# Performance work log

Measured on AMD Instinct MI355X. Metric: run time of the kernel, lower is better.

Reference implementation:

```python
import jax, jax.numpy as jnp
import numpy as np

IOU_THR = 0.5
TOP_K = 10
D_MODEL = 256
BS, NQ = 8, 1000


def _layer_norm(x, g, b, eps=1e-5):
    m = x.mean(-1, keepdims=True)
    v = ((x - m) ** 2).mean(-1, keepdims=True)
    return (x - m) * jax.lax.rsqrt(v + eps) * g + b


def _box_iou(boxes):
    # boxes: [nq, 4] xyxy; pairwise IoU [nq, nq]
    area = (boxes[:, 2] - boxes[:, 0]) * (boxes[:, 3] - boxes[:, 1])
    lt = jnp.maximum(boxes[:, None, :2], boxes[None, :, :2])
    rb = jnp.minimum(boxes[:, None, 2:], boxes[None, :, 2:])
    wh = jnp.clip(rb - lt, 0.0)
    inter = wh[..., 0] * wh[..., 1]
    union = area[:, None] + area[None, :] - inter
    return inter / union


def setup_inputs() -> dict:
    key = jax.random.key(0)
    ks = jax.random.split(key, 16)
    d = D_MODEL
    s = 1.0 / np.sqrt(d)
    tgt = jax.random.normal(ks[0], (BS, NQ, d), dtype=jnp.float32)
    seed_mask = (jax.random.uniform(ks[1], (BS, NQ, 1)) < 0.2).astype(jnp.float32)
    # cxcywh boxes in (0,1) with positive wh
    cxy = jax.random.uniform(ks[2], (BS, NQ, 2), minval=0.1, maxval=0.9)
    wh = jax.random.uniform(ks[3], (BS, NQ, 2), minval=0.05, maxval=0.3)
    pred_boxes = jnp.concatenate([cxy, wh], axis=-1).astype(jnp.float32)
    def lin(k):
        kw, kb = jax.random.split(k)
        return (jax.random.uniform(kw, (d, d), minval=-s, maxval=s, dtype=jnp.float32),
                jax.random.uniform(kb, (d,), minval=-s, maxval=s, dtype=jnp.float32))
    W1, b1 = lin(ks[4]); W2, b2 = lin(ks[5]); W3, b3 = lin(ks[6])
    W4, b4 = lin(ks[7]); W5, b5 = lin(ks[8])
    g2 = jnp.ones((d,), jnp.float32); be2 = jnp.zeros((d,), jnp.float32)
    return {"tgt": tgt, "seed_mask": seed_mask, "pred_boxes": pred_boxes,
            "W1": W1, "b1": b1, "W2": W2, "b2": b2, "g2": g2, "be2": be2,
            "W3": W3, "b3": b3, "W4": W4, "b4": b4, "W5": W5, "b5": b5}


def reference(tgt, seed_mask, pred_boxes, W1, b1, W2, b2, g2, be2, W3, b3, W4, b4, W5, b5):
    bs, nq, d = tgt.shape
    # cxcywh -> xyxy
    cxy, wh = pred_boxes[..., :2], pred_boxes[..., 2:]
    box_xyxy = jnp.concatenate([cxy - 0.5 * wh, cxy + 0.5 * wh], axis=-1)
    ious = jax.vmap(_box_iou)(box_xyxy)                       # [bs,nq,nq]
    attn_mask = ious >= IOU_THR
    neg_mask = 1.0 - seed_mask                                # [bs,nq,1]
    # mask out non-seed columns and seed rows
    overlaps = ious * jnp.swapaxes(seed_mask, 1, 2) * neg_mask  # [bs,nq,nq]
    idx = jnp.argsort(-overlaps, axis=-1)[..., :TOP_K]        # [bs,nq,k]
    nmk = jnp.take_along_axis(
        jnp.broadcast_to(jnp.swapaxes(seed_mask, 1, 2), (bs, nq, nq)), idx, axis=2)
    ious_g = jnp.take_along_axis(overlaps, idx, axis=2)       # [bs,nq,k]
    mk = nmk * (ious_g >= IOU_THR).astype(tgt.dtype)          # [bs,nq,k]
    # id token MLP + layernorm
    id_token = _layer_norm(jax.nn.relu(tgt @ W1 + b1) @ W2 + b2, g2, be2)
    # neighbor gather: [bs,nq,k,d]
    neighbors_id = jax.vmap(lambda t, i: t[i])(id_token, idx)
    id_feature = id_token[:, :, None, :] - neighbors_id
    features = jax.nn.relu(id_feature @ W3 + b3) @ W4 + b4
    cur_tgt = (features * mk[..., None]).max(axis=2)          # [bs,nq,d]
    cur_tgt = tgt + jax.nn.relu(cur_tgt @ W5 + b5) * neg_mask
    return cur_tgt, attn_mask
```

## Files before the change

kernel.cpp:

```cpp
#include <hip/hip_runtime.h>
#include <hip/hip_bf16.h>

#define BSZ   8
#define NQ    1000
#define DM    256
#define MROWS (BSZ*NQ)
#define TOPK  10

typedef __attribute__((ext_vector_type(8))) short short8;
typedef __attribute__((ext_vector_type(4))) float f32x4;
typedef unsigned short u16;

static __device__ __forceinline__ float b2f(u16 u) {
    unsigned int x = ((unsigned int)u) << 16;
    return __uint_as_float(x);
}
static __device__ __forceinline__ u16 f2b(float f) {
    __hip_bfloat16 h = __float2bfloat16(f);
    return *(u16*)&h;
}

__global__ __launch_bounds__(256) void iou_topk_k(
    const float* __restrict__ boxes, const float* __restrict__ seed,
    float* __restrict__ attn, int* __restrict__ cnt, int* __restrict__ inc0,
    int* __restrict__ idxs)
{
#pragma clang fp contract(off)
    __shared__ float sv[NQ];
    __shared__ int   sj[NQ];
    __shared__ int   scount;
    const int t   = threadIdx.x;
    const int row = blockIdx.x;
    const int b   = row / NQ;
    if (t == 0) scount = 0;

    const float* bi = boxes + (size_t)row * 4;
    const float icx = bi[0], icy = bi[1], iw = bi[2], ih = bi[3];
    const float ix0 = icx - 0.5f*iw, iy0 = icy - 0.5f*ih;
    const float ix1 = icx + 0.5f*iw, iy1 = icy + 0.5f*ih;
    const float area_i = (ix1-ix0)*(iy1-iy0);
    const float neg_i  = 1.f - seed[row];
    __syncthreads();

    float* arow = attn + (size_t)row * NQ;
    for (int j = t; j < NQ; j += 256) {
        const float* bj = boxes + (size_t)(b*NQ + j) * 4;
        const float cx = bj[0], cy = bj[1], w = bj[2], h = bj[3];
        const float x0 = cx - 0.5f*w, y0 = cy - 0.5f*h;
        const float x1 = cx + 0.5f*w, y1 = cy + 0.5f*h;
        const float area_j = (x1-x0)*(y1-y0);
        const float ltx = fmaxf(ix0, x0), lty = fmaxf(iy0, y0);
        const float rbx = fminf(ix1, x1), rby = fminf(iy1, y1);
        const float wx = fmaxf(rbx-ltx, 0.f), wy = fmaxf(rby-lty, 0.f);
        const float inter = wx*wy;
        const float uni = (area_i + area_j) - inter;
        const float iou = inter / uni;
        arow[j] = (iou >= 0.5f) ? 1.0f : 0.0f;
        const float ov = (iou * seed[b*NQ + j]) * neg_i;
        if (ov >= 0.5f) {
            const int p = atomicAdd(&scount, 1);
            if (p < NQ) { sv[p] = ov; sj[p] = j; }
        }
    }
    __syncthreads();

    if (t == 0) {
        const int n = scount;
        inc0[row] = (n < TOPK) ? 1 : 0;
        if (n <= TOPK) {
            cnt[row] = n;
            for (int k = 0; k < n; ++k) idxs[row*TOPK + k] = b*NQ + sj[k];
        } else {
            float bv[TOPK]; int bj[TOPK];
            #pragma unroll
            for (int k = 0; k < TOPK; ++k) { bv[k] = -1.f; bj[k] = 0x7fffffff; }
            for (int e = 0; e < n; ++e) {
                const float v = sv[e]; const int j = sj[e];
                int w = 0;
                #pragma unroll
                for (int k = 1; k < TOPK; ++k)
                    if (bv[k] < bv[w] || (bv[k] == bv[w] && bj[k] > bj[w])) w = k;
                if (v > bv[w] || (v == bv[w] && j < bj[w])) { bv[w] = v; bj[w] = j; }
            }
            cnt[row] = TOPK;
            for (int k = 0; k < TOPK; ++k) idxs[row*TOPK + k] = b*NQ + bj[k];
        }
    }
}

__global__ __launch_bounds__(256) void prep_w_k(
    const float* __restrict__ W1, const float* __restrict__ W2,
    const float* __restrict__ W3, const float* __restrict__ W4,
    const float* __restrict__ W5, u16* __restrict__ WT)
{
    const int m = blockIdx.y;
    const float* W = (m == 0) ? W1 : (m == 1) ? W2 : (m == 2) ? W3 : (m == 3) ? W4 : W5;
    u16* D = WT + (size_t)m * DM * DM;
    const int t  = threadIdx.x;
    const int kb = blockIdx.x * 16;
    u16 tmp[16];
    #pragma unroll
    for (int kk = 0; kk < 16; ++kk)
        tmp[kk] = f2b(W[(size_t)(kb+kk)*DM + t]);
    #pragma unroll
    for (int kk = 0; kk < 16; ++kk)
        D[(size_t)t*DM + kb + kk] = tmp[kk];
}

__global__ __launch_bounds__(256) void cvt_k(const float* __restrict__ src, u16* __restrict__ dst)
{
    const int i = (blockIdx.x * 256 + threadIdx.x) * 4;
    const float4 v = *(const float4*)&src[i];
    dst[i+0] = f2b(v.x); dst[i+1] = f2b(v.y); dst[i+2] = f2b(v.z); dst[i+3] = f2b(v.w);
}

template<int RELU, int OUT_BF16, int FINAL>
__global__ __launch_bounds__(256) void mfma_gemm_k(
    const u16* __restrict__ A, const u16* __restrict__ WT,
    const float* __restrict__ bias, void* __restrict__ Out,
    const float* __restrict__ tgt, const float* __restrict__ seed)
{
    __shared__ __align__(16) u16 A_lds[16][264];
    __shared__ __align__(16) u16 W_lds[256][72];
    const int t = threadIdx.x, r0 = blockIdx.x * 16;
    const int lane = t & 63, wave = t >> 6;
    const int m = lane & 15, quad = lane >> 4;

    #pragma unroll
    for (int it = 0; it < 2; ++it) {
        const int f = it*2048 + t*8, r = f >> 8, c = f & 255;
        *(uint4*)&A_lds[r][c] = *(const uint4*)&A[(size_t)(r0+r)*DM + c];
    }
    f32x4 acc[4];
    #pragma unroll
    for (int nt = 0; nt < 4; ++nt)
        #pragma unroll
        for (int i = 0; i < 4; ++i) acc[nt][i] = 0.f;

    for (int kc = 0; kc < 4; ++kc) {
        __syncthreads();
        #pragma unroll
        for (int pass = 0; pass < 8; ++pass) {
            const int n = pass*32 + (t >> 3), ko = (t & 7) * 8;
            *(uint4*)&W_lds[n][ko] = *(const uint4*)&WT[(size_t)n*DM + kc*64 + ko];
        }
        __syncthreads();
        #pragma unroll
        for (int ks = 0; ks < 2; ++ks) {
            const short8 a = *(const short8*)&A_lds[m][kc*64 + ks*32 + quad*8];
            #pragma unroll
            for (int nt = 0; nt < 4; ++nt) {
                const int n = wave*64 + nt*16 + m;
                const short8 b = *(const short8*)&W_lds[n][ks*32 + quad*8];
                acc[nt] = __builtin_amdgcn_mfma_f32_16x16x32_bf16(a, b, acc[nt], 0, 0, 0);
            }
        }
    }
    #pragma unroll
    for (int nt = 0; nt < 4; ++nt) {
        const int n = wave*64 + nt*16 + m;
        const float bb = bias ? bias[n] : 0.f;
        #pragma unroll
        for (int reg = 0; reg < 4; ++reg) {
            const int R = r0 + quad*4 + reg;
            float v = acc[nt][reg] + bb;
            if (RELU) v = fmaxf(v, 0.f);
            if (FINAL) v = tgt[(size_t)R*DM + n] + fmaxf(v, 0.f) * (1.f - seed[R]);
            if (OUT_BF16) ((u16*)Out)[(size_t)R*DM + n] = f2b(v);
            else          ((float*)Out)[(size_t)R*DM + n] = v;
        }
    }
}

__global__ __launch_bounds__(256) void ln_k(
    const u16* __restrict__ Y, const float* __restrict__ g,
    const float* __restrict__ be, u16* __restrict__ ID)
{
    const int wave = threadIdx.x >> 6;
    const int lane = threadIdx.x & 63;
    const int row  = blockIdx.x * 4 + wave;
    const u16* y = Y + (size_t)row * DM;
    float x[4];
    #pragma unroll
    for (int i = 0; i < 4; ++i) x[i] = b2f(y[lane + 64*i]);
    float s = x[0]+x[1]+x[2]+x[3];
    float q = x[0]*x[0]+x[1]*x[1]+x[2]*x[2]+x[3]*x[3];
    #pragma unroll
    for (int off = 32; off; off >>= 1) {
        s += __shfl_down(s, off, 64);
        q += __shfl_down(q, off, 64);
    }
    s = __shfl(s, 0, 64);
    q = __shfl(q, 0, 64);
    const float mn  = s * (1.f/DM);
    const float vr  = q * (1.f/DM) - mn*mn;
    const float inv = rsqrtf(vr + 1e-5f);
    u16* o = ID + (size_t)row * DM;
    #pragma unroll
    for (int i = 0; i < 4; ++i) {
        const int c = lane + 64*i;
        o[c] = f2b((x[i]-mn)*inv*g[c] + be[c]);
    }
}

__global__ __launch_bounds__(256) void pairs_mfma_k(
    const u16* __restrict__ P, const u16* __restrict__ W4T,
    const float* __restrict__ b3, const float* __restrict__ b4,
    const int* __restrict__ cnt, const int* __restrict__ inc0,
    const int* __restrict__ idxs, u16* __restrict__ CMAX)
{
    __shared__ __align__(16) u16 U[16][264];
    __shared__ __align__(16) u16 W_lds[256][72];
    __shared__ float cm[16][264];
    __shared__ int pl_rl[176], pl_j[176];
    __shared__ int sInc[16];
    __shared__ int np;
    const int t = threadIdx.x, r0 = blockIdx.x * 16;
    const int lane = t & 63, wave = t >> 6;
    const int m = lane & 15, quad = lane >> 4;

    if (t == 0) np = 0;
    __syncthreads();
    if (t < 16) {
        const int r = r0 + t;
        int c = cnt[r];
        c = (c < 0) ? 0 : ((c > TOPK) ? TOPK : c);
        sInc[t] = inc0[r];
        const int base = atomicAdd(&np, c);
        for (int k = 0; k < c; ++k) {
            pl_rl[base + k] = t;
            int j = idxs[r*TOPK + k];
            j = (j < 0) ? 0 : ((j >= MROWS) ? MROWS-1 : j);
            pl_j[base + k] = j;
        }
    }
    __syncthreads();
    const int npairs = np;
    #pragma unroll
    for (int rl = 0; rl < 16; ++rl)
        cm[rl][t] = sInc[rl] ? 0.f : -3.402823466e38f;

    const float bb3 = b3[t];
    float* Dl = (float*)&W_lds[0][0];

    for (int pc = 0; pc*16 < npairs; ++pc) {
        #pragma unroll
        for (int p = 0; p < 16; ++p) {
            const int pr = pc*16 + p;
            u16 uv = 0;
            if (pr < npairs) {
                const int i = r0 + pl_rl[pr];
                const int j = pl_j[pr];
                const float u = fmaxf(b2f(P[(size_t)i*DM + t]) - b2f(P[(size_t)j*DM + t]) + bb3, 0.f);
                uv = f2b(u);
            }
            U[p][t] = uv;
        }
        f32x4 acc[4];
        #pragma unroll
        for (int nt = 0; nt < 4; ++nt)
            #pragma unroll
            for (int i = 0; i < 4; ++i) acc[nt][i] = 0.f;
        for (int kc = 0; kc < 4; ++kc) {
            __syncthreads();
            #pragma unroll
            for (int pass = 0; pass < 8; ++pass) {
                const int n = pass*32 + (t >> 3), ko = (t & 7) * 8;
                *(uint4*)&W_lds[n][ko] = *(const uint4*)&W4T[(size_t)n*DM + kc*64 + ko];
            }
            __syncthreads();
            #pragma unroll
            for (int ks = 0; ks < 2; ++ks) {
                const short8 a = *(const short8*)&U[m][kc*64 + ks*32 + quad*8];
                #pragma unroll
                for (int nt = 0; nt < 4; ++nt) {
                    const int n = wave*64 + nt*16 + m;
                    const short8 b = *(const short8*)&W_lds[n][ks*32 + quad*8];
                    acc[nt] = __builtin_amdgcn_mfma_f32_16x16x32_bf16(a, b, acc[nt], 0, 0, 0);
                }
            }
        }
        __syncthreads();
        #pragma unroll
        for (int nt = 0; nt < 4; ++nt) {
            const int n = wave*64 + nt*16 + m;
            const float bb4 = b4[n];
            #pragma unroll
            for (int reg = 0; reg < 4; ++reg)
                Dl[(quad*4 + reg)*264 + n] = acc[nt][reg] + bb4;
        }
        __syncthreads();
        #pragma unroll
        for (int p = 0; p < 16; ++p) {
            const int pr = pc*16 + p;
            if (pr < npairs) {
                const int rl = pl_rl[pr];
                cm[rl][t] = fmaxf(cm[rl][t], Dl[p*264 + t]);
            }
        }
    }
    #pragma unroll
    for (int rl = 0; rl < 16; ++rl)
        CMAX[(size_t)(r0 + rl)*DM + t] = f2b(cm[rl][t]);
}

extern "C" void kernel_launch(void* const* d_in, const int* in_sizes, int n_in,
                              void* d_out, int out_size, void* d_ws, size_t ws_size,
                              hipStream_t stream)
{
    (void)in_sizes; (void)n_in; (void)out_size; (void)ws_size;
    const float* tgt   = (const float*)d_in[0];
    const float* seed  = (const float*)d_in[1];
    const float* boxes = (const float*)d_in[2];
    const float* W1 = (const float*)d_in[3];
    const float* b1 = (const float*)d_in[4];
    const float* W2 = (const float*)d_in[5];
    const float* b2 = (const float*)d_in[6];
    const float* g2 = (const float*)d_in[7];
    const float* be2= (const float*)d_in[8];
    const float* W3 = (const float*)d_in[9];
    const float* b3 = (const float*)d_in[10];
    const float* W4 = (const float*)d_in[11];
    const float* b4 = (const float*)d_in[12];
    const float* W5 = (const float*)d_in[13];
    const float* b5 = (const float*)d_in[14];

    float* out_tgt  = (float*)d_out;
    float* out_attn = out_tgt + (size_t)MROWS * DM;

    u16* WT    = (u16*)d_ws;
    u16* slotA = WT + (size_t)5*DM*DM;
    u16* slotB = slotA + (size_t)MROWS*DM;
    int* cnt   = (int*)(slotB + (size_t)MROWS*DM);
    int* inc0  = cnt + MROWS;
    int* idxs  = inc0 + MROWS;
    u16* W1T = WT;
    u16* W2T = WT + (size_t)1*DM*DM;
    u16* W3T = WT + (size_t)2*DM*DM;
    u16* W4T = WT + (size_t)3*DM*DM;
    u16* W5T = WT + (size_t)4*DM*DM;

    prep_w_k<<<dim3(16,5), 256, 0, stream>>>(W1, W2, W3, W4, W5, WT);
    cvt_k<<<MROWS*DM/1024, 256, 0, stream>>>(tgt, slotA);
    iou_topk_k<<<MROWS, 256, 0, stream>>>(boxes, seed, out_attn, cnt, inc0, idxs);
    mfma_gemm_k<1,1,0><<<MROWS/16, 256, 0, stream>>>(slotA, W1T, b1, slotB, nullptr, nullptr);
    mfma_gemm_k<0,1,0><<<MROWS/16, 256, 0, stream>>>(slotB, W2T, b2, slotA, nullptr, nullptr);
    ln_k<<<MROWS/4, 256, 0, stream>>>(slotA, g2, be2, slotB);
    mfma_gemm_k<0,1,0><<<MROWS/16, 256, 0, stream>>>(slotB, W3T, nullptr, slotA, nullptr, nullptr);
    pairs_mfma_k<<<MROWS/16, 256, 0, stream>>>(slotA, W4T, b3, b4, cnt, inc0, idxs, slotB);
    mfma_gemm_k<0,0,1><<<MROWS/16, 256, 0, stream>>>(slotB, W5T, b5, out_tgt, tgt, seed);
}
```

Measured before the change: 159.3 us.

## Fuse MLP chain, layernorm and final projection into fewer kernels via LDS

```diff
diff --git a/kernel.cpp b/kernel.cpp
--- a/kernel.cpp
+++ b/kernel.cpp
@@ -20,17 +20,36 @@
     return *(u16*)&h;
 }
 
-__global__ __launch_bounds__(256) void iou_topk_k(
+__global__ __launch_bounds__(256) void prep_iou_k(
     const float* __restrict__ boxes, const float* __restrict__ seed,
-    float* __restrict__ attn, int* __restrict__ cnt, int* __restrict__ inc0,
-    int* __restrict__ idxs)
+    const float* __restrict__ W1, const float* __restrict__ W2,
+    const float* __restrict__ W3, const float* __restrict__ W4,
+    const float* __restrict__ W5, u16* __restrict__ WT,
+    float* __restrict__ attn, int* __restrict__ cnt,
+    int* __restrict__ inc0, int* __restrict__ idxs)
 {
 #pragma clang fp contract(off)
+    if (blockIdx.x < 80) {
+        const int m  = blockIdx.x >> 4;
+        const int kb = (blockIdx.x & 15) * 16;
+        const float* W = (m==0)?W1:(m==1)?W2:(m==2)?W3:(m==3)?W4:W5;
+        u16* D = WT + (size_t)m * DM * DM;
+        const int t = threadIdx.x;
+        u16 tmp[16];
+        #pragma unroll
+        for (int kk = 0; kk < 16; ++kk)
+            tmp[kk] = f2b(W[(size_t)(kb+kk)*DM + t]);
+        #pragma unroll
+        for (int kk = 0; kk < 16; ++kk)
+            D[(size_t)t*DM + kb + kk] = tmp[kk];
+        return;
+    }
+
     __shared__ float sv[NQ];
     __shared__ int   sj[NQ];
     __shared__ int   scount;
     const int t   = threadIdx.x;
-    const int row = blockIdx.x;
+    const int row = blockIdx.x - 80;
     const int b   = row / NQ;
     if (t == 0) scount = 0;
 
@@ -88,55 +107,21 @@
     }
 }
 
-__global__ __launch_bounds__(256) void prep_w_k(
-    const float* __restrict__ W1, const float* __restrict__ W2,
-    const float* __restrict__ W3, const float* __restrict__ W4,
-    const float* __restrict__ W5, u16* __restrict__ WT)
-{
-    const int m = blockIdx.y;
-    const float* W = (m == 0) ? W1 : (m == 1) ? W2 : (m == 2) ? W3 : (m == 3) ? W4 : W5;
-    u16* D = WT + (size_t)m * DM * DM;
-    const int t  = threadIdx.x;
-    const int kb = blockIdx.x * 16;
-    u16 tmp[16];
-    #pragma unroll
-    for (int kk = 0; kk < 16; ++kk)
-        tmp[kk] = f2b(W[(size_t)(kb+kk)*DM + t]);
-    #pragma unroll
-    for (int kk = 0; kk < 16; ++kk)
-        D[(size_t)t*DM + kb + kk] = tmp[kk];
-}
-
-__global__ __launch_bounds__(256) void cvt_k(const float* __restrict__ src, u16* __restrict__ dst)
-{
-    const int i = (blockIdx.x * 256 + threadIdx.x) * 4;
-    const float4 v = *(const float4*)&src[i];
-    dst[i+0] = f2b(v.x); dst[i+1] = f2b(v.y); dst[i+2] = f2b(v.z); dst[i+3] = f2b(v.w);
-}
-
-template<int RELU, int OUT_BF16, int FINAL>
-__global__ __launch_bounds__(256) void mfma_gemm_k(
-    const u16* __restrict__ A, const u16* __restrict__ WT,
-    const float* __restrict__ bias, void* __restrict__ Out,
-    const float* __restrict__ tgt, const float* __restrict__ seed)
-{
-    __shared__ __align__(16) u16 A_lds[16][264];
-    __shared__ __align__(16) u16 W_lds[256][72];
-    const int t = threadIdx.x, r0 = blockIdx.x * 16;
+template<int EPI>
+static __device__ __forceinline__ void block_gemm256(
+    const u16 (*__restrict__ A)[264], const u16* __restrict__ WT,
+    const float* __restrict__ bias, u16 (*__restrict__ OutL)[264],
+    u16* __restrict__ OutG, float* __restrict__ OutF,
+    const float* __restrict__ tgt, const float* __restrict__ seed,
+    int r0, u16 (*__restrict__ W_lds)[72], int t)
+{
     const int lane = t & 63, wave = t >> 6;
     const int m = lane & 15, quad = lane >> 4;
-
-    #pragma unroll
-    for (int it = 0; it < 2; ++it) {
-        const int f = it*2048 + t*8, r = f >> 8, c = f & 255;
-        *(uint4*)&A_lds[r][c] = *(const uint4*)&A[(size_t)(r0+r)*DM + c];
-    }
     f32x4 acc[4];
     #pragma unroll
     for (int nt = 0; nt < 4; ++nt)
         #pragma unroll
         for (int i = 0; i < 4; ++i) acc[nt][i] = 0.f;
-
     for (int kc = 0; kc < 4; ++kc) {
         __syncthreads();
         #pragma unroll
@@ -147,7 +132,7 @@
         __syncthreads();
         #pragma unroll
         for (int ks = 0; ks < 2; ++ks) {
-            const short8 a = *(const short8*)&A_lds[m][kc*64 + ks*32 + quad*8];
+            const short8 a = *(const short8*)&A[m][kc*64 + ks*32 + quad*8];
             #pragma unroll
             for (int nt = 0; nt < 4; ++nt) {
                 const int n = wave*64 + nt*16 + m;
@@ -162,52 +147,85 @@
         const float bb = bias ? bias[n] : 0.f;
         #pragma unroll
         for (int reg = 0; reg < 4; ++reg) {
-            const int R = r0 + quad*4 + reg;
+            const int rl = quad*4 + reg;
             float v = acc[nt][reg] + bb;
-            if (RELU) v = fmaxf(v, 0.f);
-            if (FINAL) v = tgt[(size_t)R*DM + n] + fmaxf(v, 0.f) * (1.f - seed[R]);
-            if (OUT_BF16) ((u16*)Out)[(size_t)R*DM + n] = f2b(v);
-            else          ((float*)Out)[(size_t)R*DM + n] = v;
-        }
-    }
-}
-
-__global__ __launch_bounds__(256) void ln_k(
-    const u16* __restrict__ Y, const float* __restrict__ g,
-    const float* __restrict__ be, u16* __restrict__ ID)
-{
-    const int wave = threadIdx.x >> 6;
-    const int lane = threadIdx.x & 63;
-    const int row  = blockIdx.x * 4 + wave;
-    const u16* y = Y + (size_t)row * DM;
-    float x[4];
-    #pragma unroll
-    for (int i = 0; i < 4; ++i) x[i] = b2f(y[lane + 64*i]);
-    float s = x[0]+x[1]+x[2]+x[3];
-    float q = x[0]*x[0]+x[1]*x[1]+x[2]*x[2]+x[3]*x[3];
-    #pragma unroll
-    for (int off = 32; off; off >>= 1) {
-        s += __shfl_down(s, off, 64);
-        q += __shfl_down(q, off, 64);
-    }
-    s = __shfl(s, 0, 64);
-    q = __shfl(q, 0, 64);
-    const float mn  = s * (1.f/DM);
-    const float vr  = q * (1.f/DM) - mn*mn;
-    const float inv = rsqrtf(vr + 1e-5f);
-    u16* o = ID + (size_t)row * DM;
-    #pragma unroll
-    for (int i = 0; i < 4; ++i) {
-        const int c = lane + 64*i;
-        o[c] = f2b((x[i]-mn)*inv*g[c] + be[c]);
-    }
-}
-
-__global__ __launch_bounds__(256) void pairs_mfma_k(
-    const u16* __restrict__ P, const u16* __restrict__ W4T,
+            if (EPI == 0) OutL[rl][n] = f2b(fmaxf(v, 0.f));
+            if (EPI == 1) OutL[rl][n] = f2b(v);
+            if (EPI == 2) OutG[(size_t)(r0+rl)*DM + n] = f2b(v);
+            if (EPI == 3) {
+                const int R = r0 + rl;
+                OutF[(size_t)R*DM + n] = tgt[(size_t)R*DM + n]
+                                       + fmaxf(v, 0.f) * (1.f - seed[R]);
+            }
+        }
+    }
+}
+
+__global__ __launch_bounds__(256) void mlp_k(
+    const float* __restrict__ tgt, const u16* __restrict__ WT,
+    const float* __restrict__ b1, const float* __restrict__ b2,
+    const float* __restrict__ g2, const float* __restrict__ be2,
+    u16* __restrict__ P)
+{
+    __shared__ __align__(16) u16 bufA[16][264];
+    __shared__ __align__(16) u16 bufB[16][264];
+    __shared__ __align__(16) u16 W_lds[256][72];
+    const int t = threadIdx.x, r0 = blockIdx.x * 16;
+    const int lane = t & 63, wave = t >> 6;
+
+    {
+        const int r = t >> 4, c0 = (t & 15) * 16;
+        const float* src = &tgt[(size_t)(r0 + r)*DM + c0];
+        u16 h[16];
+        #pragma unroll
+        for (int q = 0; q < 4; ++q) {
+            const float4 f = *(const float4*)&src[q*4];
+            h[q*4+0] = f2b(f.x); h[q*4+1] = f2b(f.y);
+            h[q*4+2] = f2b(f.z); h[q*4+3] = f2b(f.w);
+        }
+        *(uint4*)&bufA[r][c0]     = *(uint4*)&h[0];
+        *(uint4*)&bufA[r][c0 + 8] = *(uint4*)&h[8];
+    }
+    const u16* W1T = WT;
+    const u16* W2T = WT + (size_t)1*DM*DM;
+    const u16* W3T = WT + (size_t)2*DM*DM;
+
+    block_gemm256<0>(bufA, W1T, b1, bufB, nullptr, nullptr, nullptr, nullptr, r0, W_lds, t);
+    block_gemm256<1>(bufB, W2T, b2, bufA, nullptr, nullptr, nullptr, nullptr, r0, W_lds, t);
+    __syncthreads();
+    for (int rr = 0; rr < 4; ++rr) {
+        const int row = wave*4 + rr;
+        float x[4];
+        #pragma unroll
+        for (int i = 0; i < 4; ++i) x[i] = b2f(bufA[row][lane + 64*i]);
+        float s = x[0]+x[1]+x[2]+x[3];
+        float q = x[0]*x[0]+x[1]*x[1]+x[2]*x[2]+x[3]*x[3];
+        #pragma unroll
+        for (int off = 32; off; off >>= 1) {
+            s += __shfl_down(s, off, 64);
+            q += __shfl_down(q, off, 64);
+        }
+        s = __shfl(s, 0, 64); q = __shfl(q, 0, 64);
+        const float mn  = s * (1.f/DM);
+        const float vr  = q * (1.f/DM) - mn*mn;
+        const float inv = rsqrtf(vr + 1e-5f);
+        #pragma unroll
+        for (int i = 0; i < 4; ++i) {
+            const int c = lane + 64*i;
+            bufA[row][c] = f2b((x[i]-mn)*inv*g2[c] + be2[c]);
+        }
+    }
+    block_gemm256<2>(bufA, W3T, nullptr, nullptr, P, nullptr, nullptr, nullptr, r0, W_lds, t);
+}
+
+__global__ __launch_bounds__(256) void pairs_final_k(
+    const u16* __restrict__ P, const u16* __restrict__ WT,
     const float* __restrict__ b3, const float* __restrict__ b4,
+    const float* __restrict__ b5,
     const int* __restrict__ cnt, const int* __restrict__ inc0,
-    const int* __restrict__ idxs, u16* __restrict__ CMAX)
+    const int* __restrict__ idxs,
+    const float* __restrict__ tgt, const float* __restrict__ seed,
+    float* __restrict__ out)
 {
     __shared__ __align__(16) u16 U[16][264];
     __shared__ __align__(16) u16 W_lds[256][72];
@@ -218,6 +236,8 @@
     const int t = threadIdx.x, r0 = blockIdx.x * 16;
     const int lane = t & 63, wave = t >> 6;
     const int m = lane & 15, quad = lane >> 4;
+    const u16* W4T = WT + (size_t)3*DM*DM;
+    const u16* W5T = WT + (size_t)4*DM*DM;
 
     if (t == 0) np = 0;
     __syncthreads();
@@ -301,7 +321,8 @@
     }
     #pragma unroll
     for (int rl = 0; rl < 16; ++rl)
-        CMAX[(size_t)(r0 + rl)*DM + t] = f2b(cm[rl][t]);
+        U[rl][t] = f2b(cm[rl][t]);
+    block_gemm256<3>(U, W5T, b5, nullptr, nullptr, out, tgt, seed, r0, W_lds, t);
 }
 
 extern "C" void kernel_launch(void* const* d_in, const int* in_sizes, int n_in,
@@ -328,25 +349,15 @@
     float* out_tgt  = (float*)d_out;
     float* out_attn = out_tgt + (size_t)MROWS * DM;
 
-    u16* WT    = (u16*)d_ws;
-    u16* slotA = WT + (size_t)5*DM*DM;
-    u16* slotB = slotA + (size_t)MROWS*DM;
-    int* cnt   = (int*)(slotB + (size_t)MROWS*DM);
-    int* inc0  = cnt + MROWS;
-    int* idxs  = inc0 + MROWS;
-    u16* W1T = WT;
-    u16* W2T = WT + (size_t)1*DM*DM;
-    u16* W3T = WT + (size_t)2*DM*DM;
-    u16* W4T = WT + (size_t)3*DM*DM;
-    u16* W5T = WT + (size_t)4*DM*DM;
-
-    prep_w_k<<<dim3(16,5), 256, 0, stream>>>(W1, W2, W3, W4, W5, WT);
-    cvt_k<<<MROWS*DM/1024, 256, 0, stream>>>(tgt, slotA);
-    iou_topk_k<<<MROWS, 256, 0, stream>>>(boxes, seed, out_attn, cnt, inc0, idxs);
-    mfma_gemm_k<1,1,0><<<MROWS/16, 256, 0, stream>>>(slotA, W1T, b1, slotB, nullptr, nullptr);
-    mfma_gemm_k<0,1,0><<<MROWS/16, 256, 0, stream>>>(slotB, W2T, b2, slotA, nullptr, nullptr);
-    ln_k<<<MROWS/4, 256, 0, stream>>>(slotA, g2, be2, slotB);
-    mfma_gemm_k<0,1,0><<<MROWS/16, 256, 0, stream>>>(slotB, W3T, nullptr, slotA, nullptr, nullptr);
-    pairs_mfma_k<<<MROWS/16, 256, 0, stream>>>(slotA, W4T, b3, b4, cnt, inc0, idxs, slotB);
-    mfma_gemm_k<0,0,1><<<MROWS/16, 256, 0, stream>>>(slotB, W5T, b5, out_tgt, tgt, seed);
-}
+    u16* WT   = (u16*)d_ws;
+    u16* P    = WT + (size_t)5*DM*DM;
+    int* cnt  = (int*)(P + (size_t)MROWS*DM);
+    int* inc0 = cnt + MROWS;
+    int* idxs = inc0 + MROWS;
+
+    prep_iou_k<<<80 + MROWS, 256, 0, stream>>>(boxes, seed, W1, W2, W3, W4, W5,
+                                               WT, out_attn, cnt, inc0, idxs);
+    mlp_k<<<MROWS/16, 256, 0, stream>>>(tgt, WT, b1, b2, g2, be2, P);
+    pairs_final_k<<<MROWS/16, 256, 0, stream>>>(P, WT, b3, b4, b5, cnt, inc0, idxs,
+                                                tgt, seed, out_tgt);
+}
```

Result: faster. 142.4 us (-10.6%).
